# Kernel tuning notes

Hardware: AMD Instinct MI355X
Metric: run time of the kernel (lower is better)

Reference implementation:

```python
import jax, jax.numpy as jnp
import numpy as np

B, M, D, H = 2, 2048, 1024, 16
DH = D // H            # 64 head dim
R_ATTN = 512           # rank of q/k/v SVD factors
FFN_D = 2048           # GEGLU inner dim; Wi out = 2*FFN_D
R_FFN = 1024           # rank of FFN SVD factors
ROPE_BASE = 10000.0
LN_EPS = 1e-5


def _layernorm(x, g, b):
    mu = jnp.mean(x, axis=-1, keepdims=True)
    var = jnp.mean(jnp.square(x - mu), axis=-1, keepdims=True)
    return (x - mu) * jax.lax.rsqrt(var + LN_EPS) * g + b


def _rotate_half(x):
    x1, x2 = jnp.split(x, 2, axis=-1)
    return jnp.concatenate((-x2, x1), axis=-1)


def _rope_cos_sin(m, dh, dtype):
    inv_freq = 1.0 / (ROPE_BASE ** (jnp.arange(0, dh, 2, dtype=jnp.float32) / dh))
    freqs = jnp.arange(m, dtype=jnp.float32)[:, None] * inv_freq[None, :]  # [M, dh/2]
    emb = jnp.concatenate((freqs, freqs), axis=-1)  # [M, dh]
    return jnp.cos(emb).astype(dtype), jnp.sin(emb).astype(dtype)


def setup_inputs() -> dict:
    key = jax.random.key(0)
    ks = iter(jax.random.split(key, 32))
    rn = lambda shape, s: jax.random.normal(next(ks), shape, jnp.float32) * s
    w = 0.02
    return {
        'hidden_states': rn((B, M, D), 1.0),
        'ln1_g': jnp.ones((D,), jnp.float32), 'ln1_b': jnp.zeros((D,), jnp.float32),
        'Uq': rn((D, R_ATTN), w), 'Vq': rn((R_ATTN, D), w), 'bq': rn((D,), w),
        'Uk': rn((D, R_ATTN), w), 'Vk': rn((R_ATTN, D), w), 'bk': rn((D,), w),
        'Uv': rn((D, R_ATTN), w), 'Vv': rn((R_ATTN, D), w), 'bv': rn((D,), w),
        'Wo': rn((D, D), w), 'bo': rn((D,), w),  # dense attn out proj, torch [out,in]
        'ln2_g': jnp.ones((D,), jnp.float32), 'ln2_b': jnp.zeros((D,), jnp.float32),
        'U1': rn((D, R_FFN), w), 'V1': rn((R_FFN, 2 * FFN_D), w), 'b1': rn((2 * FFN_D,), w),
        'U2': rn((FFN_D, R_FFN), w), 'V2': rn((R_FFN, D), w), 'b2': rn((D,), w),
    }


def reference(hidden_states, ln1_g, ln1_b, Uq, Vq, bq, Uk, Vk, bk, Uv, Vv, bv,
              Wo, bo, ln2_g, ln2_b, U1, V1, b1, U2, V2, b2):
    x = hidden_states
    xn = _layernorm(x, ln1_g, ln1_b)
    # low-rank QKV: y = (x @ U) @ V + b
    q = (xn @ Uq) @ Vq + bq
    k = (xn @ Uk) @ Vk + bk
    v = (xn @ Uv) @ Vv + bv
    to_bhmd = lambda t: t.reshape(B, M, H, DH).transpose(0, 2, 1, 3)
    q, k, v = to_bhmd(q), to_bhmd(k), to_bhmd(v)
    cos, sin = _rope_cos_sin(M, DH, q.dtype)  # [M, DH]
    q = q * cos + _rotate_half(q) * sin
    k = k * cos + _rotate_half(k) * sin
    scale = 1.0 / np.sqrt(DH)
    scores = jnp.einsum('bhmd,bhnd->bhmn', q, k) * scale  # [B,H,M,M]
    attn = jax.nn.softmax(scores, axis=-1)
    out = jnp.einsum('bhmn,bhnd->bhmd', attn, v)
    out = out.transpose(0, 2, 1, 3).reshape(B, M, D)
    x = x + out @ Wo.T + bo
    # low-rank GEGLU FFN
    xn2 = _layernorm(x, ln2_g, ln2_b)
    z = (xn2 @ U1) @ V1 + b1  # [B,M,2*FFN_D]
    z1, z2 = jnp.split(z, 2, axis=-1)
    h = jax.nn.gelu(z1, approximate=True) * z2  # GEGLU, tanh approx
    y = (h @ U2) @ V2 + b2
    return x + y
```

## Files before the change

kernel.cpp:

```cpp
#include <hip/hip_runtime.h>


typedef unsigned short u16;
typedef unsigned int u32;
typedef u16 u16x8 __attribute__((ext_vector_type(8)));
typedef __bf16 bf16x8 __attribute__((ext_vector_type(8)));
typedef float f32x4 __attribute__((ext_vector_type(4)));

__device__ __forceinline__ u16 f2bf(float f) {
    u32 u = __builtin_bit_cast(u32, f);
    u += 0x7fff + ((u >> 16) & 1);
    return (u16)(u >> 16);
}
__device__ __forceinline__ u16 f2bf_t(float f) {
    return (u16)(__builtin_bit_cast(u32, f) >> 16);
}
__device__ __forceinline__ float bf2f(u16 h) {
    u32 u = ((u32)h) << 16;
    return __builtin_bit_cast(float, u);
}

__device__ __forceinline__ void gload16(const void* g, void* l) {
    __builtin_amdgcn_global_load_lds(
        (const __attribute__((address_space(1))) void*)g,
        (__attribute__((address_space(3))) void*)l, 16, 0, 0);
}

#define BARRIER_LGKM() __asm__ volatile("s_waitcnt lgkmcnt(0)\ns_barrier" ::: "memory")

template <int CTRL>
__device__ __forceinline__ float dppror(float x) {
    return __builtin_bit_cast(float,
        __builtin_amdgcn_mov_dpp(__builtin_bit_cast(int, x), CTRL, 0xF, 0xF, true));
}
__device__ __forceinline__ float rowsum16(float x) {
    x += dppror<0x128>(x);
    x += dppror<0x124>(x);
    x += dppror<0x122>(x);
    x += dppror<0x121>(x);
    return x;
}

#define MB 1048576u
#define OFF_UQKVT (0*MB)
#define OFF_VQKVT (3*MB)
#define OFF_WOB   (6*MB)
#define OFF_U1T   (8*MB)
#define OFF_V1TP  (10*MB)
#define OFF_U2T   (18*MB)
#define OFF_V2T   (22*MB)
#define OFF_BQKV  (24*MB)
#define OFF_B1P   (24*MB + 16384u)
#define OFF_XN    (25*MB)
#define OFF_TBUF  (33*MB)
#define OFF_QB    (45*MB)
#define OFF_KB    (53*MB)
#define OFF_HB    (45*MB)
#define OFF_VTB   (61*MB)
#define OFF_OB    (69*MB)
#define OFF_X2    (93*MB)

__global__ __launch_bounds__(256) void transpose_bf16_kernel(
    const float* __restrict__ in, u16* __restrict__ out, int K, int N)
{
    __shared__ float tile[32][33];
    int tx = threadIdx.x & 31, ty = threadIdx.x >> 5;
    int n0 = blockIdx.x * 32, k0 = blockIdx.y * 32;
    for (int i = 0; i < 4; i++)
        tile[ty + i*8][tx] = in[(size_t)(k0 + ty + i*8) * N + n0 + tx];
    __syncthreads();
    for (int i = 0; i < 4; i++)
        out[(size_t)(n0 + ty + i*8) * K + k0 + tx] = f2bf(tile[tx][ty + i*8]);
}

__global__ __launch_bounds__(256) void transpose_geglu_kernel(
    const float* __restrict__ in, u16* __restrict__ out)
{
    __shared__ float tile[32][33];
    int tx = threadIdx.x & 31, ty = threadIdx.x >> 5;
    int n0 = blockIdx.x * 32, k0 = blockIdx.y * 32;
    int g = n0 >> 5;
    int src = (tx < 16) ? (g*16 + tx) : (2048 + g*16 + (tx - 16));
    for (int i = 0; i < 4; i++)
        tile[ty + i*8][tx] = in[(size_t)(k0 + ty + i*8) * 4096 + src];
    __syncthreads();
    for (int i = 0; i < 4; i++)
        out[(size_t)(n0 + ty + i*8) * 1024 + k0 + tx] = f2bf(tile[tx][ty + i*8]);
}

__global__ __launch_bounds__(256) void convert_bf16_kernel(
    const float* __restrict__ in, u16* __restrict__ out, int n)
{
    int id = blockIdx.x * blockDim.x + threadIdx.x;
    int i4 = id * 4;
    if (i4 < n) {
        float4 v = *(const float4*)(in + i4);
        u16 tmp[4] = {f2bf(v.x), f2bf(v.y), f2bf(v.z), f2bf(v.w)};
        *(uint2*)(out + i4) = *(const uint2*)tmp;
    }
}

__global__ __launch_bounds__(256) void biascat_kernel(
    const float* __restrict__ a, const float* __restrict__ b,
    const float* __restrict__ c, float* __restrict__ o,
    const float* __restrict__ b1, float* __restrict__ b1p)
{
    int id = blockIdx.x * 256 + threadIdx.x;
    if (id < 3072) {
        float v = (id < 1024) ? a[id] : (id < 2048 ? b[id - 1024] : c[id - 2048]);
        o[id] = v;
    }
    int g = id >> 5, s = id & 31;
    b1p[id] = b1[(s < 16) ? (g*16 + s) : (2048 + g*16 + (s - 16))];
}

__global__ __launch_bounds__(256) void ln_kernel(
    const float* __restrict__ x, const float* __restrict__ g,
    const float* __restrict__ bta, u16* __restrict__ out)
{
    int w = threadIdx.x >> 6, lane = threadIdx.x & 63;
    int row = blockIdx.x * 4 + w;
    const float* xr = x + (size_t)row * 1024;
    float vals[16];
    float s = 0.f, s2 = 0.f;
    #pragma unroll
    for (int ii = 0; ii < 16; ii++) {
        float v = xr[lane + ii*64];
        vals[ii] = v; s += v; s2 += v * v;
    }
    #pragma unroll
    for (int off = 1; off < 64; off <<= 1) {
        s  += __shfl_xor(s, off);
        s2 += __shfl_xor(s2, off);
    }
    float mu = s * (1.f/1024.f);
    float var = s2 * (1.f/1024.f) - mu * mu;
    float rs = rsqrtf(var + 1e-5f);
    #pragma unroll
    for (int ii = 0; ii < 16; ii++) {
        int col = lane + ii*64;
        out[(size_t)row * 1024 + col] = f2bf((vals[ii] - mu) * rs * g[col] + bta[col]);
    }
}

__global__ __launch_bounds__(256) void gemm_bt_kernel(
    const u16* __restrict__ A, int lda, const u16* __restrict__ Bt,
    void* __restrict__ Cout, int ldc, const float* __restrict__ bias,
    const float* __restrict__ resid, int Kdim, int mode)
{
    __shared__ u16 As[2][4096];
    __shared__ u16 Bs[2][4096];
    int tid = threadIdx.x;
    int m0 = blockIdx.y * 128, n0 = blockIdx.x * 128;
    int w = tid >> 6, lane = tid & 63, quad = lane >> 4, l15 = lane & 15;
    int wm = (w >> 1) * 64, wn = (w & 1) * 64;
    int sr = tid >> 2, sc8 = (tid & 3) * 8;

    f32x4 acc[4][4] = {};

    const u16* Ap = A  + (size_t)(m0 + sr) * lda  + sc8;
    const u16* Bp = Bt + (size_t)(n0 + sr) * Kdim + sc8;

    uint4 a0 = *(const uint4*)Ap;
    uint4 a1 = *(const uint4*)(Ap + (size_t)64 * lda);
    uint4 b0 = *(const uint4*)Bp;
    uint4 b1v = *(const uint4*)(Bp + (size_t)64 * Kdim);
    *(uint4*)&As[0][sr * 32 + sc8]        = a0;
    *(uint4*)&As[0][(sr + 64) * 32 + sc8] = a1;
    *(uint4*)&Bs[0][sr * 32 + sc8]        = b0;
    *(uint4*)&Bs[0][(sr + 64) * 32 + sc8] = b1v;
    BARRIER_LGKM();

    for (int k0 = 0; k0 < Kdim; k0 += 32) {
        int cur = (k0 >> 5) & 1;
        bool more = (k0 + 32) < Kdim;
        if (more) {
            a0  = *(const uint4*)(Ap + k0 + 32);
            a1  = *(const uint4*)(Ap + k0 + 32 + (size_t)64 * lda);
            b0  = *(const uint4*)(Bp + k0 + 32);
            b1v = *(const uint4*)(Bp + k0 + 32 + (size_t)64 * Kdim);
        }
        const u16* Asc = As[cur];
        const u16* Bsc = Bs[cur];
        bf16x8 af[4], bfr[4];
        #pragma unroll
        for (int i = 0; i < 4; i++)
            af[i] = *(const bf16x8*)&Asc[(wm + i*16 + l15) * 32 + quad * 8];
        #pragma unroll
        for (int j = 0; j < 4; j++)
            bfr[j] = *(const bf16x8*)&Bsc[(wn + j*16 + l15) * 32 + quad * 8];
        #pragma unroll
        for (int i = 0; i < 4; i++)
            #pragma unroll
            for (int j = 0; j < 4; j++)
                acc[i][j] = __builtin_amdgcn_mfma_f32_16x16x32_bf16(af[i], bfr[j], acc[i][j], 0, 0, 0);
        if (more) {
            int nxt = cur ^ 1;
            *(uint4*)&As[nxt][sr * 32 + sc8]        = a0;
            *(uint4*)&As[nxt][(sr + 64) * 32 + sc8] = a1;
            *(uint4*)&Bs[nxt][sr * 32 + sc8]        = b0;
            *(uint4*)&Bs[nxt][(sr + 64) * 32 + sc8] = b1v;
            BARRIER_LGKM();
        }
    }

    if (mode == 2) {
        u16* hb = (u16*)Cout;
        #pragma unroll
        for (int i = 0; i < 4; i++) {
            int row = m0 + wm + i*16 + quad*4;
            #pragma unroll
            for (int p = 0; p < 2; p++) {
                int colz = n0 + wn + p*32 + l15;
                float bz1 = bias[colz], bz2 = bias[colz + 16];
                int hcol = ((n0 + wn) >> 1) + p*16 + l15;
                #pragma unroll
                for (int r = 0; r < 4; r++) {
                    float z1 = acc[i][2*p][r] + bz1;
                    float z2 = acc[i][2*p+1][r] + bz2;
                    float uu = 0.7978845608028654f * (z1 + 0.044715f * z1 * z1 * z1);
                    float e = __expf(2.f * uu);
                    float th = (e - 1.f) / (e + 1.f);
                    float hv = 0.5f * z1 * (1.f + th) * z2;
                    hb[(size_t)(row + r) * ldc + hcol] = f2bf(hv);
                }
            }
        }
        return;
    }
    #pragma unroll
    for (int i = 0; i < 4; i++) {
        int row = m0 + wm + i*16 + quad*4;
        #pragma unroll
        for (int j = 0; j < 4; j++) {
            int col = n0 + wn + j*16 + l15;
            float bv = bias ? bias[col] : 0.f;
            #pragma unroll
            for (int r = 0; r < 4; r++) {
                float v = acc[i][j][r] + bv;
                size_t idx = (size_t)(row + r) * ldc + col;
                if (mode == 0) ((float*)Cout)[idx] = v + resid[idx];
                else           ((u16*)Cout)[idx] = f2bf(v);
            }
        }
    }
}

__global__ __launch_bounds__(256) void qkv2_kernel(
    const u16* __restrict__ T, const u16* __restrict__ Vw,
    const float* __restrict__ bqkv, u16* __restrict__ qout,
    u16* __restrict__ kout, u16* __restrict__ vtout)
{
    __shared__ u16 As[2][4096];
    __shared__ u16 Bs[2][4096];
    int tid = threadIdx.x;
    int z = blockIdx.z;
    int m0 = blockIdx.y * 128, n0 = blockIdx.x * 128;
    int w = tid >> 6, lane = tid & 63, quad = lane >> 4, l15 = lane & 15;
    int wm = (w >> 1) * 64, wn = (w & 1) * 64;
    int sr = tid >> 2, sc8 = (tid & 3) * 8;

    f32x4 acc[4][4] = {};

    const u16* Ap = T  + (size_t)z * 512 + (size_t)(m0 + sr) * 1536 + sc8;
    const u16* Bp = Vw + (size_t)z * 512 * 1024 + (size_t)(n0 + sr) * 512 + sc8;

    uint4 a0 = *(const uint4*)Ap;
    uint4 a1 = *(const uint4*)(Ap + (size_t)64 * 1536);
    uint4 b0 = *(const uint4*)Bp;
    uint4 b1v = *(const uint4*)(Bp + (size_t)64 * 512);
    *(uint4*)&As[0][sr * 32 + sc8]        = a0;
    *(uint4*)&As[0][(sr + 64) * 32 + sc8] = a1;
    *(uint4*)&Bs[0][sr * 32 + sc8]        = b0;
    *(uint4*)&Bs[0][(sr + 64) * 32 + sc8] = b1v;
    BARRIER_LGKM();

    for (int k0 = 0; k0 < 512; k0 += 32) {
        int cur = (k0 >> 5) & 1;
        bool more = (k0 + 32) < 512;
        if (more) {
            a0  = *(const uint4*)(Ap + k0 + 32);
            a1  = *(const uint4*)(Ap + k0 + 32 + (size_t)64 * 1536);
            b0  = *(const uint4*)(Bp + k0 + 32);
            b1v = *(const uint4*)(Bp + k0 + 32 + (size_t)64 * 512);
        }
        const u16* Asc = As[cur];
        const u16* Bsc = Bs[cur];
        bf16x8 af[4], bfr[4];
        #pragma unroll
        for (int i = 0; i < 4; i++)
            af[i] = *(const bf16x8*)&Asc[(wm + i*16 + l15) * 32 + quad * 8];
        #pragma unroll
        for (int j = 0; j < 4; j++)
            bfr[j] = *(const bf16x8*)&Bsc[(wn + j*16 + l15) * 32 + quad * 8];
        #pragma unroll
        for (int i = 0; i < 4; i++)
            #pragma unroll
            for (int j = 0; j < 4; j++)
                acc[i][j] = __builtin_amdgcn_mfma_f32_16x16x32_bf16(af[i], bfr[j], acc[i][j], 0, 0, 0);
        if (more) {
            int nxt = cur ^ 1;
            *(uint4*)&As[nxt][sr * 32 + sc8]        = a0;
            *(uint4*)&As[nxt][(sr + 64) * 32 + sc8] = a1;
            *(uint4*)&Bs[nxt][sr * 32 + sc8]        = b0;
            *(uint4*)&Bs[nxt][(sr + 64) * 32 + sc8] = b1v;
            BARRIER_LGKM();
        }
    }

    const float* bias = bqkv + z * 1024;
    if (z < 2) {
        u16* Ob = z ? kout : qout;
        float qscale = z ? 1.f : 0.18033688011112042f;
        #pragma unroll
        for (int i = 0; i < 4; i++) {
            int row0 = m0 + wm + i*16 + quad*4;
            #pragma unroll
            for (int j = 0; j < 2; j++) {
                int col = n0 + wn + j*16 + l15;
                float bj = bias[col], bj2 = bias[col + 32];
                float invf = exp2f((float)(col & 31) * -0.4152410118609203f);
                #pragma unroll
                for (int r = 0; r < 4; r++) {
                    int t = row0 + r;
                    float fr = (float)(t & 2047) * invf;
                    float sn, cs;
                    __sincosf(fr, &sn, &cs);
                    sn *= qscale; cs *= qscale;
                    float v1 = acc[i][j][r] + bj;
                    float v2 = acc[i][j+2][r] + bj2;
                    Ob[(size_t)t * 1024 + col]      = f2bf(v1 * cs - v2 * sn);
                    Ob[(size_t)t * 1024 + col + 32] = f2bf(v2 * cs + v1 * sn);
                }
            }
        }
    } else {
        int bb = m0 >> 11;
        #pragma unroll
        for (int i = 0; i < 4; i++) {
            int row0 = m0 + wm + i*16 + quad*4;
            #pragma unroll
            for (int j = 0; j < 4; j++) {
                int col = n0 + wn + j*16 + l15;
                float bj = bias[col];
                u16 pack[4];
                #pragma unroll
                for (int r = 0; r < 4; r++) pack[r] = f2bf(acc[i][j][r] + bj);
                size_t dst = ((size_t)(bb * 16 + (col >> 6)) * 64 + (col & 63)) * 2048 + (row0 & 2047);
                *(uint2*)&vtout[dst] = *(const uint2*)pack;
            }
        }
    }
}

__global__ __launch_bounds__(256) void attn_kernel(
    const u16* __restrict__ Q, const u16* __restrict__ K,
    const u16* __restrict__ Vt, u16* __restrict__ O)
{
    __shared__ u16 Ks[2][64 * 64];
    __shared__ u16 Vs[2][64 * 64];
    __shared__ u16 Ps[128 * 72];
    int tid = threadIdx.x;
    int bh = blockIdx.x;
    int b = bh >> 4, h = bh & 15;
    int m0 = blockIdx.y * 128;
    int w = tid >> 6, lane = tid & 63, quad = lane >> 4, l15 = lane & 15;
    int wm = w * 32;
    size_t qkbase = (size_t)b * 2048 * 1024 + h * 64;
    const u16* Vg = Vt + (size_t)bh * 64 * 2048;

    bf16x8 qf[2][2];
    #pragma unroll
    for (int i = 0; i < 2; i++)
        #pragma unroll
        for (int ks = 0; ks < 2; ks++)
            qf[i][ks] = *(const bf16x8*)(Q + qkbase +
                (size_t)(m0 + wm + i*16 + l15) * 1024 + ks*32 + quad*8);

    f32x4 oacc[2][4] = {};
    float lsum[2][4] = {};

    int r0 = tid >> 3, p = tid & 7;
    int c0 = (p ^ (r0 & 7)) * 8;
    int xsw = l15 & 7;

    #define STAGE(buf, key0) do {                                               \
        gload16(K + qkbase + (size_t)((key0) + r0) * 1024 + c0,                 \
                &Ks[buf][r0 * 64 + p * 8]);                                     \
        gload16(K + qkbase + (size_t)((key0) + r0 + 32) * 1024 + c0,            \
                &Ks[buf][(r0 + 32) * 64 + p * 8]);                              \
        gload16(Vg + (size_t)r0 * 2048 + (key0) + c0,                           \
                &Vs[buf][r0 * 64 + p * 8]);                                     \
        gload16(Vg + (size_t)(r0 + 32) * 2048 + (key0) + c0,                    \
                &Vs[buf][(r0 + 32) * 64 + p * 8]);                              \
    } while (0)

    STAGE(0, 0);
    __syncthreads();

    for (int kt = 0; kt < 32; kt++) {
        int cur = kt & 1;
        if (kt < 31) STAGE(cur ^ 1, (kt + 1) * 64);
        const u16* Ksc = Ks[cur];
        const u16* Vsc = Vs[cur];

        f32x4 sacc[2][4] = {};
        #pragma unroll
        for (int ks = 0; ks < 2; ks++) {
            bf16x8 kf[4];
            #pragma unroll
            for (int j = 0; j < 4; j++)
                kf[j] = *(const bf16x8*)&Ksc[(j*16 + l15) * 64 + (((ks*4 + quad) ^ xsw) * 8)];
            #pragma unroll
            for (int i = 0; i < 2; i++)
                #pragma unroll
                for (int j = 0; j < 4; j++)
                    sacc[i][j] = __builtin_amdgcn_mfma_f32_16x16x32_bf16(qf[i][ks], kf[j], sacc[i][j], 0, 0, 0);
        }

        #pragma unroll
        for (int i = 0; i < 2; i++) {
            int prow0 = (wm + i*16 + quad*4) * 72;
            #pragma unroll
            for (int r = 0; r < 4; r++) {
                float p0 = __builtin_amdgcn_exp2f(sacc[i][0][r]);
                float p1 = __builtin_amdgcn_exp2f(sacc[i][1][r]);
                float p2 = __builtin_amdgcn_exp2f(sacc[i][2][r]);
                float p3 = __builtin_amdgcn_exp2f(sacc[i][3][r]);
                lsum[i][r] += (p0 + p1) + (p2 + p3);
                int pr = prow0 + r * 72;
                Ps[pr + l15]      = f2bf_t(p0);
                Ps[pr + 16 + l15] = f2bf_t(p1);
                Ps[pr + 32 + l15] = f2bf_t(p2);
                Ps[pr + 48 + l15] = f2bf_t(p3);
            }
        }

        #pragma unroll
        for (int ks = 0; ks < 2; ks++) {
            bf16x8 pf[2], vf[4];
            #pragma unroll
            for (int i = 0; i < 2; i++)
                pf[i] = *(const bf16x8*)&Ps[(wm + i*16 + l15) * 72 + ks*32 + quad*8];
            #pragma unroll
            for (int j = 0; j < 4; j++)
                vf[j] = *(const bf16x8*)&Vsc[(j*16 + l15) * 64 + (((ks*4 + quad) ^ xsw) * 8)];
            #pragma unroll
            for (int i = 0; i < 2; i++)
                #pragma unroll
                for (int j = 0; j < 4; j++)
                    oacc[i][j] = __builtin_amdgcn_mfma_f32_16x16x32_bf16(pf[i], vf[j], oacc[i][j], 0, 0, 0);
        }
        __syncthreads();
    }

    #pragma unroll
    for (int i = 0; i < 2; i++)
        #pragma unroll
        for (int r = 0; r < 4; r++) {
            float inv = 1.f / rowsum16(lsum[i][r]);
            int row = m0 + wm + i*16 + quad*4 + r;
            #pragma unroll
            for (int j = 0; j < 4; j++)
                O[qkbase + (size_t)row * 1024 + j*16 + l15] = f2bf(oacc[i][j][r] * inv);
        }
}

extern "C" void kernel_launch(void* const* d_in, const int* in_sizes, int n_in,
                              void* d_out, int out_size, void* d_ws, size_t ws_size,
                              hipStream_t stream) {
    (void)in_sizes; (void)n_in; (void)out_size; (void)ws_size;
    const float* x     = (const float*)d_in[0];
    const float* ln1_g = (const float*)d_in[1];
    const float* ln1_b = (const float*)d_in[2];
    const float* Uq    = (const float*)d_in[3];
    const float* Vq    = (const float*)d_in[4];
    const float* bq    = (const float*)d_in[5];
    const float* Uk    = (const float*)d_in[6];
    const float* Vk    = (const float*)d_in[7];
    const float* bk    = (const float*)d_in[8];
    const float* Uv    = (const float*)d_in[9];
    const float* Vv    = (const float*)d_in[10];
    const float* bv    = (const float*)d_in[11];
    const float* Wo    = (const float*)d_in[12];
    const float* bo    = (const float*)d_in[13];
    const float* ln2_g = (const float*)d_in[14];
    const float* ln2_b = (const float*)d_in[15];
    const float* U1    = (const float*)d_in[16];
    const float* V1    = (const float*)d_in[17];
    const float* b1    = (const float*)d_in[18];
    const float* U2    = (const float*)d_in[19];
    const float* V2    = (const float*)d_in[20];
    const float* b2    = (const float*)d_in[21];
    float* out = (float*)d_out;
    char* ws = (char*)d_ws;

    u16* UQKVT = (u16*)(ws + OFF_UQKVT);
    u16* VQKVT = (u16*)(ws + OFF_VQKVT);
    u16* WOB   = (u16*)(ws + OFF_WOB);
    u16* U1T   = (u16*)(ws + OFF_U1T);
    u16* V1TP  = (u16*)(ws + OFF_V1TP);
    u16* U2T   = (u16*)(ws + OFF_U2T);
    u16* V2T   = (u16*)(ws + OFF_V2T);
    float* BQKV = (float*)(ws + OFF_BQKV);
    float* B1P  = (float*)(ws + OFF_B1P);
    u16* xn  = (u16*)(ws + OFF_XN);
    u16* tbuf= (u16*)(ws + OFF_TBUF);
    u16* qb  = (u16*)(ws + OFF_QB);
    u16* kb  = (u16*)(ws + OFF_KB);
    u16* vtb = (u16*)(ws + OFF_VTB);
    u16* ob  = (u16*)(ws + OFF_OB);
    u16* hb  = (u16*)(ws + OFF_HB);
    float* x2 = (float*)(ws + OFF_X2);

    transpose_bf16_kernel<<<dim3(16, 32), 256, 0, stream>>>(Uq, UQKVT,             1024, 512);
    transpose_bf16_kernel<<<dim3(16, 32), 256, 0, stream>>>(Uk, UQKVT + 512*1024,  1024, 512);
    transpose_bf16_kernel<<<dim3(16, 32), 256, 0, stream>>>(Uv, UQKVT + 1024*1024, 1024, 512);
    transpose_bf16_kernel<<<dim3(32, 16), 256, 0, stream>>>(Vq, VQKVT,            512, 1024);
    transpose_bf16_kernel<<<dim3(32, 16), 256, 0, stream>>>(Vk, VQKVT + 524288,   512, 1024);
    transpose_bf16_kernel<<<dim3(32, 16), 256, 0, stream>>>(Vv, VQKVT + 1048576,  512, 1024);
    convert_bf16_kernel<<<1024, 256, 0, stream>>>(Wo, WOB, 1024 * 1024);
    transpose_bf16_kernel<<<dim3(32, 32), 256, 0, stream>>>(U1, U1T, 1024, 1024);
    transpose_geglu_kernel<<<dim3(128, 32), 256, 0, stream>>>(V1, V1TP);
    transpose_bf16_kernel<<<dim3(32, 64), 256, 0, stream>>>(U2, U2T, 2048, 1024);
    transpose_bf16_kernel<<<dim3(32, 32), 256, 0, stream>>>(V2, V2T, 1024, 1024);
    biascat_kernel<<<16, 256, 0, stream>>>(bq, bk, bv, BQKV, b1, B1P);

    ln_kernel<<<1024, 256, 0, stream>>>(x, ln1_g, ln1_b, xn);

    gemm_bt_kernel<<<dim3(12, 32), 256, 0, stream>>>(xn, 1024, UQKVT, tbuf, 1536,
                                                     nullptr, nullptr, 1024, 1);
    qkv2_kernel<<<dim3(8, 32, 3), 256, 0, stream>>>(tbuf, VQKVT, BQKV, qb, kb, vtb);

    attn_kernel<<<dim3(32, 16), 256, 0, stream>>>(qb, kb, vtb, ob);

    gemm_bt_kernel<<<dim3(8, 32), 256, 0, stream>>>(ob, 1024, WOB, x2, 1024,
                                                    bo, x, 1024, 0);
    ln_kernel<<<1024, 256, 0, stream>>>(x2, ln2_g, ln2_b, xn);

    gemm_bt_kernel<<<dim3(8, 32), 256, 0, stream>>>(xn, 1024, U1T, tbuf, 1024,
                                                    nullptr, nullptr, 1024, 1);
    gemm_bt_kernel<<<dim3(32, 32), 256, 0, stream>>>(tbuf, 1024, V1TP, hb, 2048,
                                                     B1P, nullptr, 1024, 2);
    gemm_bt_kernel<<<dim3(8, 32), 256, 0, stream>>>(hb, 2048, U2T, tbuf, 1024,
                                                    nullptr, nullptr, 2048, 1);
    gemm_bt_kernel<<<dim3(8, 32), 256, 0, stream>>>(tbuf, 1024, V2T, out, 1024,
                                                    b2, x2, 1024, 0);
}
```

Baseline: 502.3 us.

## Merge weight-prep launches into one kernel and use direct global-to-LDS loads in GEMMs

Replaces the twelve separate transpose, convert and bias-concat launches with a single prep kernel that dispatches work by block index range, cutting per-launch overhead. Separately, the GEMM and QKV second-stage kernels now stage tiles with global_load_lds directly into shared memory instead of loading into registers and then storing to LDS, and synchronise with __syncthreads each iteration. The LDS layout changes from row-stride indexing to linear tid*8 placement, which matches the previous layout only when each row of 32 elements maps to 4 consecutive threads. The added per-iteration barrier may reduce overlap between loads and compute.

```diff
diff --git a/kernel.cpp b/kernel.cpp
--- a/kernel.cpp
+++ b/kernel.cpp
@@ -25,8 +25,6 @@
         (const __attribute__((address_space(1))) void*)g,
         (__attribute__((address_space(3))) void*)l, 16, 0, 0);
 }
-
-#define BARRIER_LGKM() __asm__ volatile("s_waitcnt lgkmcnt(0)\ns_barrier" ::: "memory")
 
 template <int CTRL>
 __device__ __forceinline__ float dppror(float x) {
@@ -60,58 +58,62 @@
 #define OFF_OB    (69*MB)
 #define OFF_X2    (93*MB)
 
-__global__ __launch_bounds__(256) void transpose_bf16_kernel(
-    const float* __restrict__ in, u16* __restrict__ out, int K, int N)
+__global__ __launch_bounds__(256) void prep_kernel(
+    const float* __restrict__ Uq, const float* __restrict__ Uk,
+    const float* __restrict__ Uv, const float* __restrict__ Vq,
+    const float* __restrict__ Vk, const float* __restrict__ Vv,
+    const float* __restrict__ Wo, const float* __restrict__ U1,
+    const float* __restrict__ V1, const float* __restrict__ U2,
+    const float* __restrict__ V2,
+    const float* __restrict__ bq, const float* __restrict__ bk,
+    const float* __restrict__ bv, const float* __restrict__ b1,
+    u16* __restrict__ UQKVT, u16* __restrict__ VQKVT, u16* __restrict__ WOB,
+    u16* __restrict__ U1T, u16* __restrict__ V1TP, u16* __restrict__ U2T,
+    u16* __restrict__ V2T, float* __restrict__ BQKV, float* __restrict__ B1P)
 {
     __shared__ float tile[32][33];
+    int bid = blockIdx.x;
+
+    if (bid >= 12288) {
+        int id = (bid - 12288) * 256 + threadIdx.x;
+        if (id < 3072) {
+            float v = (id < 1024) ? bq[id] : (id < 2048 ? bk[id - 1024] : bv[id - 2048]);
+            BQKV[id] = v;
+        }
+        int g = id >> 5, s = id & 31;
+        B1P[id] = b1[(s < 16) ? (g*16 + s) : (2048 + g*16 + (s - 16))];
+        return;
+    }
+    if (bid >= 11264) {
+        int i4 = ((bid - 11264) * 256 + threadIdx.x) * 4;
+        float4 v = *(const float4*)(Wo + i4);
+        u16 tmp[4] = {f2bf(v.x), f2bf(v.y), f2bf(v.z), f2bf(v.w)};
+        *(uint2*)(WOB + i4) = *(const uint2*)tmp;
+        return;
+    }
+
+    const float* src; u16* dst; int K, N, src_ld, nx; bool gg = false;
+    if (bid < 3072) {
+        int t = bid / 512; bid -= t * 512;
+        if (t < 3) { src = t==0 ? Uq : (t==1 ? Uk : Uv);
+                     dst = UQKVT + t * 512*1024; K = 1024; N = 512; src_ld = 512; nx = 16; }
+        else { int z = t - 3; src = z==0 ? Vq : (z==1 ? Vk : Vv);
+               dst = VQKVT + z * 524288; K = 512; N = 1024; src_ld = 1024; nx = 32; }
+    } else if (bid < 4096)  { src = U1; dst = U1T;  K = 1024; N = 1024; src_ld = 1024; nx = 32;  bid -= 3072; }
+    else if (bid < 8192)    { src = V1; dst = V1TP; K = 1024; N = 4096; src_ld = 4096; nx = 128; bid -= 4096; gg = true; }
+    else if (bid < 10240)   { src = U2; dst = U2T;  K = 2048; N = 1024; src_ld = 1024; nx = 32;  bid -= 8192; }
+    else                    { src = V2; dst = V2T;  K = 1024; N = 1024; src_ld = 1024; nx = 32;  bid -= 10240; }
+
     int tx = threadIdx.x & 31, ty = threadIdx.x >> 5;
-    int n0 = blockIdx.x * 32, k0 = blockIdx.y * 32;
+    int n0 = (bid % nx) * 32, k0 = (bid / nx) * 32;
+    int srccol;
+    if (gg) { int g = n0 >> 5; srccol = (tx < 16) ? (g*16 + tx) : (2048 + g*16 + (tx - 16)); }
+    else srccol = n0 + tx;
     for (int i = 0; i < 4; i++)
-        tile[ty + i*8][tx] = in[(size_t)(k0 + ty + i*8) * N + n0 + tx];
+        tile[ty + i*8][tx] = src[(size_t)(k0 + ty + i*8) * src_ld + srccol];
     __syncthreads();
     for (int i = 0; i < 4; i++)
-        out[(size_t)(n0 + ty + i*8) * K + k0 + tx] = f2bf(tile[tx][ty + i*8]);
-}
-
-__global__ __launch_bounds__(256) void transpose_geglu_kernel(
-    const float* __restrict__ in, u16* __restrict__ out)
-{
-    __shared__ float tile[32][33];
-    int tx = threadIdx.x & 31, ty = threadIdx.x >> 5;
-    int n0 = blockIdx.x * 32, k0 = blockIdx.y * 32;
-    int g = n0 >> 5;
-    int src = (tx < 16) ? (g*16 + tx) : (2048 + g*16 + (tx - 16));
-    for (int i = 0; i < 4; i++)
-        tile[ty + i*8][tx] = in[(size_t)(k0 + ty + i*8) * 4096 + src];
-    __syncthreads();
-    for (int i = 0; i < 4; i++)
-        out[(size_t)(n0 + ty + i*8) * 1024 + k0 + tx] = f2bf(tile[tx][ty + i*8]);
-}
-
-__global__ __launch_bounds__(256) void convert_bf16_kernel(
-    const float* __restrict__ in, u16* __restrict__ out, int n)
-{
-    int id = blockIdx.x * blockDim.x + threadIdx.x;
-    int i4 = id * 4;
-    if (i4 < n) {
-        float4 v = *(const float4*)(in + i4);
-        u16 tmp[4] = {f2bf(v.x), f2bf(v.y), f2bf(v.z), f2bf(v.w)};
-        *(uint2*)(out + i4) = *(const uint2*)tmp;
-    }
-}
-
-__global__ __launch_bounds__(256) void biascat_kernel(
-    const float* __restrict__ a, const float* __restrict__ b,
-    const float* __restrict__ c, float* __restrict__ o,
-    const float* __restrict__ b1, float* __restrict__ b1p)
-{
-    int id = blockIdx.x * 256 + threadIdx.x;
-    if (id < 3072) {
-        float v = (id < 1024) ? a[id] : (id < 2048 ? b[id - 1024] : c[id - 2048]);
-        o[id] = v;
-    }
-    int g = id >> 5, s = id & 31;
-    b1p[id] = b1[(s < 16) ? (g*16 + s) : (2048 + g*16 + (s - 16))];
+        dst[(size_t)(n0 + ty + i*8) * K + k0 + tx] = f2bf(tile[tx][ty + i*8]);
 }
 
 __global__ __launch_bounds__(256) void ln_kernel(
@@ -161,25 +163,19 @@
     const u16* Ap = A  + (size_t)(m0 + sr) * lda  + sc8;
     const u16* Bp = Bt + (size_t)(n0 + sr) * Kdim + sc8;
 
-    uint4 a0 = *(const uint4*)Ap;
-    uint4 a1 = *(const uint4*)(Ap + (size_t)64 * lda);
-    uint4 b0 = *(const uint4*)Bp;
-    uint4 b1v = *(const uint4*)(Bp + (size_t)64 * Kdim);
-    *(uint4*)&As[0][sr * 32 + sc8]        = a0;
-    *(uint4*)&As[0][(sr + 64) * 32 + sc8] = a1;
-    *(uint4*)&Bs[0][sr * 32 + sc8]        = b0;
-    *(uint4*)&Bs[0][(sr + 64) * 32 + sc8] = b1v;
-    BARRIER_LGKM();
+    #define GSTAGE(buf, koff) do {                                        \
+        gload16(Ap + (koff),                     &As[buf][tid * 8]);      \
+        gload16(Ap + (koff) + (size_t)64 * lda,  &As[buf][2048 + tid*8]); \
+        gload16(Bp + (koff),                     &Bs[buf][tid * 8]);      \
+        gload16(Bp + (koff) + (size_t)64 * Kdim, &Bs[buf][2048 + tid*8]); \
+    } while (0)
+
+    GSTAGE(0, 0);
+    __syncthreads();
 
     for (int k0 = 0; k0 < Kdim; k0 += 32) {
         int cur = (k0 >> 5) & 1;
-        bool more = (k0 + 32) < Kdim;
-        if (more) {
-            a0  = *(const uint4*)(Ap + k0 + 32);
-            a1  = *(const uint4*)(Ap + k0 + 32 + (size_t)64 * lda);
-            b0  = *(const uint4*)(Bp + k0 + 32);
-            b1v = *(const uint4*)(Bp + k0 + 32 + (size_t)64 * Kdim);
-        }
+        if (k0 + 32 < Kdim) GSTAGE(cur ^ 1, k0 + 32);
         const u16* Asc = As[cur];
         const u16* Bsc = Bs[cur];
         bf16x8 af[4], bfr[4];
@@ -194,15 +190,9 @@
             #pragma unroll
             for (int j = 0; j < 4; j++)
                 acc[i][j] = __builtin_amdgcn_mfma_f32_16x16x32_bf16(af[i], bfr[j], acc[i][j], 0, 0, 0);
-        if (more) {
-            int nxt = cur ^ 1;
-            *(uint4*)&As[nxt][sr * 32 + sc8]        = a0;
-            *(uint4*)&As[nxt][(sr + 64) * 32 + sc8] = a1;
-            *(uint4*)&Bs[nxt][sr * 32 + sc8]        = b0;
-            *(uint4*)&Bs[nxt][(sr + 64) * 32 + sc8] = b1v;
-            BARRIER_LGKM();
-        }
-    }
+        __syncthreads();
+    }
+    #undef GSTAGE
 
     if (mode == 2) {
         u16* hb = (u16*)Cout;
@@ -265,25 +255,19 @@
     const u16* Ap = T  + (size_t)z * 512 + (size_t)(m0 + sr) * 1536 + sc8;
     const u16* Bp = Vw + (size_t)z * 512 * 1024 + (size_t)(n0 + sr) * 512 + sc8;
 
-    uint4 a0 = *(const uint4*)Ap;
-    uint4 a1 = *(const uint4*)(Ap + (size_t)64 * 1536);
-    uint4 b0 = *(const uint4*)Bp;
-    uint4 b1v = *(const uint4*)(Bp + (size_t)64 * 512);
-    *(uint4*)&As[0][sr * 32 + sc8]        = a0;
-    *(uint4*)&As[0][(sr + 64) * 32 + sc8] = a1;
-    *(uint4*)&Bs[0][sr * 32 + sc8]        = b0;
-    *(uint4*)&Bs[0][(sr + 64) * 32 + sc8] = b1v;
-    BARRIER_LGKM();
+    #define QSTAGE(buf, koff) do {                                        \
+        gload16(Ap + (koff),                     &As[buf][tid * 8]);      \
+        gload16(Ap + (koff) + (size_t)64 * 1536, &As[buf][2048 + tid*8]); \
+        gload16(Bp + (koff),                     &Bs[buf][tid * 8]);      \
+        gload16(Bp + (koff) + (size_t)64 * 512,  &Bs[buf][2048 + tid*8]); \
+    } while (0)
+
+    QSTAGE(0, 0);
+    __syncthreads();
 
     for (int k0 = 0; k0 < 512; k0 += 32) {
         int cur = (k0 >> 5) & 1;
-        bool more = (k0 + 32) < 512;
-        if (more) {
-            a0  = *(const uint4*)(Ap + k0 + 32);
-            a1  = *(const uint4*)(Ap + k0 + 32 + (size_t)64 * 1536);
-            b0  = *(const uint4*)(Bp + k0 + 32);
-            b1v = *(const uint4*)(Bp + k0 + 32 + (size_t)64 * 512);
-        }
+        if (k0 + 32 < 512) QSTAGE(cur ^ 1, k0 + 32);
         const u16* Asc = As[cur];
         const u16* Bsc = Bs[cur];
         bf16x8 af[4], bfr[4];
@@ -298,15 +282,9 @@
             #pragma unroll
             for (int j = 0; j < 4; j++)
                 acc[i][j] = __builtin_amdgcn_mfma_f32_16x16x32_bf16(af[i], bfr[j], acc[i][j], 0, 0, 0);
-        if (more) {
-            int nxt = cur ^ 1;
-            *(uint4*)&As[nxt][sr * 32 + sc8]        = a0;
-            *(uint4*)&As[nxt][(sr + 64) * 32 + sc8] = a1;
-            *(uint4*)&Bs[nxt][sr * 32 + sc8]        = b0;
-            *(uint4*)&Bs[nxt][(sr + 64) * 32 + sc8] = b1v;
-            BARRIER_LGKM();
-        }
-    }
+        __syncthreads();
+    }
+    #undef QSTAGE
 
     const float* bias = bqkv + z * 1024;
     if (z < 2) {
@@ -453,6 +431,7 @@
         }
         __syncthreads();
     }
+    #undef STAGE
 
     #pragma unroll
     for (int i = 0; i < 2; i++)
@@ -513,18 +492,9 @@
     u16* hb  = (u16*)(ws + OFF_HB);
     float* x2 = (float*)(ws + OFF_X2);
 
-    transpose_bf16_kernel<<<dim3(16, 32), 256, 0, stream>>>(Uq, UQKVT,             1024, 512);
-    transpose_bf16_kernel<<<dim3(16, 32), 256, 0, stream>>>(Uk, UQKVT + 512*1024,  1024, 512);
-    transpose_bf16_kernel<<<dim3(16, 32), 256, 0, stream>>>(Uv, UQKVT + 1024*1024, 1024, 512);
-    transpose_bf16_kernel<<<dim3(32, 16), 256, 0, stream>>>(Vq, VQKVT,            512, 1024);
-    transpose_bf16_kernel<<<dim3(32, 16), 256, 0, stream>>>(Vk, VQKVT + 524288,   512, 1024);
-    transpose_bf16_kernel<<<dim3(32, 16), 256, 0, stream>>>(Vv, VQKVT + 1048576,  512, 1024);
-    convert_bf16_kernel<<<1024, 256, 0, stream>>>(Wo, WOB, 1024 * 1024);
-    transpose_bf16_kernel<<<dim3(32, 32), 256, 0, stream>>>(U1, U1T, 1024, 1024);
-    transpose_geglu_kernel<<<dim3(128, 32), 256, 0, stream>>>(V1, V1TP);
-    transpose_bf16_kernel<<<dim3(32, 64), 256, 0, stream>>>(U2, U2T, 2048, 1024);
-    transpose_bf16_kernel<<<dim3(32, 32), 256, 0, stream>>>(V2, V2T, 1024, 1024);
-    biascat_kernel<<<16, 256, 0, stream>>>(bq, bk, bv, BQKV, b1, B1P);
+    prep_kernel<<<12304, 256, 0, stream>>>(
+        Uq, Uk, Uv, Vq, Vk, Vv, Wo, U1, V1, U2, V2, bq, bk, bv, b1,
+        UQKVT, VQKVT, WOB, U1T, V1TP, U2T, V2T, BQKV, B1P);
 
     ln_kernel<<<1024, 256, 0, stream>>>(x, ln1_g, ln1_b, xn);
 
```

New measurement: 468.9 us. -6.6%, faster.
